# Kernel optimization log

Measured on AMD Instinct MI355X. Metric: run time of the kernel, lower is better.

Reference implementation:

```python
import jax, jax.numpy as jnp
import numpy as np

N = 50000      # nodes
E = 800000     # edges
IN = 128       # in_dim
H = 128        # hidden_dim
OUT = 64       # out_dim
B = 6          # block_num
NEG_SLOPE = 0.01  # nn.LeakyReLU default


def setup_inputs() -> dict:
    key = jax.random.key(0)
    ks = jax.random.split(key, 10)
    s = 0.05
    return {
        "inputs": jax.random.normal(ks[0], (N, IN), jnp.float32),
        "edges": jax.random.randint(ks[1], (2, E), 0, N, jnp.int32),
        "w_in": jax.random.normal(ks[2], (IN, H), jnp.float32) * s,
        "b_in": jnp.zeros((H,), jnp.float32),
        "w1": jax.random.normal(ks[3], (B, H, H), jnp.float32) * s,
        "b1": jnp.zeros((B, H), jnp.float32),
        "w2": jax.random.normal(ks[4], (B, H, H), jnp.float32) * s,
        "b2": jnp.zeros((B, H), jnp.float32),
        "w_out": jax.random.normal(ks[5], (H, OUT), jnp.float32) * s,
        "b_out": jnp.zeros((OUT,), jnp.float32),
    }


def _leaky(x):
    return jnp.where(x >= 0, x, NEG_SLOPE * x)


def _gcn_conv(x, W, b, src, dst, norm):
    # GCNConv: out = D^{-1/2}(A+I)D^{-1/2} (x W) + b, with self-loops folded in.
    xw = x @ W                                   # [N, d_out]
    msg = xw[src] * norm[src, None]              # gather + edge scaling [E, d_out]
    agg = jax.ops.segment_sum(msg, dst, num_segments=N)
    agg = agg * norm[:, None] + xw * (norm * norm)[:, None]  # neighbors + self-loop
    return agg + b


def reference(inputs, edges, w_in, b_in, w1, b1, w2, b2, w_out, b_out):
    src, dst = edges[0], edges[1]
    deg = 1.0 + jax.ops.segment_sum(jnp.ones((E,), inputs.dtype), dst, num_segments=N)
    norm = jax.lax.rsqrt(deg)                    # [N]

    x = _leaky(_gcn_conv(inputs, w_in, b_in, src, dst, norm))
    for i in range(B):  # fixed small layer loop (structurally distinct params)
        h = _leaky(_gcn_conv(x, w1[i], b1[i], src, dst, norm))
        h = _leaky(_gcn_conv(h, w2[i], b2[i], src, dst, norm))
        x = (x + h) * 0.5
    # dropout in eval mode -> identity
    x_out = _gcn_conv(x, w_out, b_out, src, dst, norm)
    return (x_out, x)
```

## Files before the change

### kernel.cpp

```cpp
#include <hip/hip_runtime.h>

#define NNODES 50000
#define NPAD   50048
#define NEDGES 800000
#define HDIM 128
#define OUTDIM 64

#define GEMM_GRID 391
#define GEMM_BLK  512
#define GEMM_TILES (NPAD / 16)

typedef short short8 __attribute__((ext_vector_type(8)));
typedef _Float16 half8 __attribute__((ext_vector_type(8)));
typedef _Float16 half4 __attribute__((ext_vector_type(4)));
typedef float f32x4 __attribute__((ext_vector_type(4)));
typedef float f32x8 __attribute__((ext_vector_type(8)));

__device__ __forceinline__ unsigned short f2bf(float f) {
    unsigned int u = __builtin_bit_cast(unsigned int, f);
    unsigned int r = (u + 0x7FFFu + ((u >> 16) & 1u)) >> 16;
    return (unsigned short)r;
}
__device__ __forceinline__ float bf2f(unsigned short b) {
    unsigned int u = ((unsigned int)b) << 16;
    return __builtin_bit_cast(float, u);
}

__global__ void count_kernel(const int* __restrict__ dst, int* __restrict__ deg,
                             int* __restrict__ epos) {
    int e = blockIdx.x * 256 + threadIdx.x;
    if (e < NEDGES) epos[e] = atomicAdd(&deg[dst[e]], 1);
}

__global__ __launch_bounds__(256) void bsum_kernel(const int* __restrict__ deg,
                                                   int* __restrict__ bsum) {
    __shared__ int red[256];
    int i = blockIdx.x * 256 + threadIdx.x;
    red[threadIdx.x] = (i < NNODES) ? deg[i] : 0;
    __syncthreads();
    for (int off = 128; off; off >>= 1) {
        if (threadIdx.x < off) red[threadIdx.x] += red[threadIdx.x + off];
        __syncthreads();
    }
    if (threadIdx.x == 0) bsum[blockIdx.x] = red[0];
}

__global__ __launch_bounds__(256) void bscan_kernel(const int* __restrict__ bsum,
                                                    int* __restrict__ bofs) {
    __shared__ int s[256];
    int t = threadIdx.x;
    int v = (t < 196) ? bsum[t] : 0;
    s[t] = v;
    __syncthreads();
    for (int off = 1; off < 256; off <<= 1) {
        int u = (t >= off) ? s[t - off] : 0;
        __syncthreads();
        s[t] += u;
        __syncthreads();
    }
    if (t < 196) bofs[t] = s[t] - v;
}

__global__ __launch_bounds__(256) void emit_kernel(
    const int* __restrict__ deg, const int* __restrict__ bofs,
    int* __restrict__ row_ptr, float* __restrict__ norm) {
    __shared__ int s[256];
    int t = threadIdx.x;
    int i = blockIdx.x * 256 + t;
    int v = (i < NNODES) ? deg[i] : 0;
    s[t] = v;
    __syncthreads();
    for (int off = 1; off < 256; off <<= 1) {
        int u = (t >= off) ? s[t - off] : 0;
        __syncthreads();
        s[t] += u;
        __syncthreads();
    }
    int excl = s[t] - v + bofs[blockIdx.x];
    if (i < NNODES) {
        row_ptr[i] = excl;
        norm[i] = rsqrtf(1.0f + (float)v);
    }
    if (i == NNODES - 1) row_ptr[NNODES] = NEDGES;
}

__global__ void fill_kernel(const int* __restrict__ src, const int* __restrict__ dst,
                            const int* __restrict__ epos, const int* __restrict__ row_ptr,
                            int* __restrict__ sorted_src) {
    int e = blockIdx.x * 256 + threadIdx.x;
    if (e < NEDGES) sorted_src[row_ptr[dst[e]] + epos[e]] = src[e];
}

__global__ __launch_bounds__(256) void prep_w_kernel(
    const float* __restrict__ w_in, const float* __restrict__ w1,
    const float* __restrict__ w2, const float* __restrict__ w_out,
    unsigned short* __restrict__ wT, _Float16* __restrict__ w2f) {
    int idx = blockIdx.x * 256 + threadIdx.x;
    if (idx < 16384 + 98304) {
        const float* W;
        unsigned short* o;
        int e;
        if (idx < 16384) {
            W = w_in; o = wT; e = idx;
        } else {
            int j = idx - 16384; int m = j >> 14; e = j & 16383;
            W = w1 + ((size_t)m << 14); o = wT + (size_t)(1 + m) * 32768;
        }
        int k = e >> 7, n = e & 127;
        float v = W[e];
        unsigned short h = f2bf(v);
        o[(size_t)n * 256 + k] = h;
        o[(size_t)n * 256 + 128 + k] = f2bf(v - bf2f(h));
    } else if (idx < 16384 + 196608) {
        int j = idx - 16384 - 98304; int m = j >> 14; int e = j & 16383;
        int k = e >> 7, n = e & 127;
        w2f[(size_t)m * 16384 + n * 128 + k] = (_Float16)w2[((size_t)m << 14) + e];
    } else {
        int e = idx - 212992;
        int k = e >> 6, n = e & 63;
        float v = w_out[e];
        unsigned short h = f2bf(v);
        unsigned short* o = wT + (size_t)7 * 32768;
        o[(size_t)n * 256 + k] = h;
        o[(size_t)n * 256 + 128 + k] = f2bf(v - bf2f(h));
    }
}

__global__ __launch_bounds__(256) void split_x_kernel(
    const float* __restrict__ x, unsigned short* __restrict__ xc) {
    int gid = blockIdx.x * 256 + threadIdx.x;
    int row = gid >> 6;
    int kk = (gid & 63) * 2;
    float2 v = {0.f, 0.f};
    if (row < NNODES) v = *(const float2*)(x + (size_t)row * 128 + kk);
    unsigned short h0 = f2bf(v.x), h1 = f2bf(v.y);
    unsigned short l0 = f2bf(v.x - bf2f(h0)), l1 = f2bf(v.y - bf2f(h1));
    *(unsigned int*)(xc + (size_t)row * 256 + kk) =
        (unsigned int)h0 | ((unsigned int)h1 << 16);
    *(unsigned int*)(xc + (size_t)row * 256 + 128 + kk) =
        (unsigned int)l0 | ((unsigned int)l1 << 16);
}

template <int NCOLS>
__global__ __launch_bounds__(GEMM_BLK) void gemm_bf_kernel(
    const unsigned short* __restrict__ xc, const unsigned short* __restrict__ wT,
    const float* __restrict__ norm, _Float16* __restrict__ y) {
    __shared__ unsigned short Blds[NCOLS * 256];
    const int t = threadIdx.x;
    const int wave = t >> 6, lane = t & 63, quad = lane >> 4, l16 = lane & 15;

    constexpr int NCH = NCOLS * 32;
#pragma unroll
    for (int i = 0; i < NCH / GEMM_BLK; ++i) {
        int C = i * GEMM_BLK + t;
        int n = C >> 5, c = C & 31;
        const unsigned short* gp = wT + ((size_t)n << 8) + ((c ^ (n & 7)) << 3);
        unsigned short* lp = Blds + ((size_t)C << 3);
        __builtin_amdgcn_global_load_lds(
            (const __attribute__((address_space(1))) void*)gp,
            (__attribute__((address_space(3))) void*)lp, 16, 0, 0);
    }
    __syncthreads();

    const int wid = blockIdx.x * (GEMM_BLK / 64) + wave;
    const int sw = l16 & 7;
    const int rb0 = wid * 16;

    short8 a0[8];
    const unsigned short* ap0 = xc + ((size_t)(rb0 + l16) << 8) + quad * 8;
#pragma unroll
    for (int ck = 0; ck < 8; ++ck) a0[ck] = *(const short8*)(ap0 + ck * 32);

    float nm0[4];
#pragma unroll
    for (int r = 0; r < 4; ++r) {
        int r0 = rb0 + quad * 4 + r;
        nm0[r] = norm[r0 < NNODES ? r0 : 0];
    }

#pragma unroll
    for (int nt = 0; nt < NCOLS / 16; ++nt) {
        const unsigned short* bp = Blds + ((size_t)(nt * 16 + l16) << 8);
        short8 bh[4], bl[4];
#pragma unroll
        for (int ck = 0; ck < 4; ++ck) {
            bh[ck] = *(const short8*)(bp + (((ck * 4 + quad) ^ sw) << 3));
            bl[ck] = *(const short8*)(bp + (((16 + ck * 4 + quad) ^ sw) << 3));
        }
        f32x4 ac0 = (f32x4){0.f, 0.f, 0.f, 0.f};
#pragma unroll
        for (int ck = 0; ck < 4; ++ck) {
            ac0 = __builtin_amdgcn_mfma_f32_16x16x32_bf16(a0[ck], bh[ck], ac0, 0, 0, 0);
            ac0 = __builtin_amdgcn_mfma_f32_16x16x32_bf16(a0[ck], bl[ck], ac0, 0, 0, 0);
            ac0 = __builtin_amdgcn_mfma_f32_16x16x32_bf16(a0[4 + ck], bh[ck], ac0, 0, 0, 0);
        }
        int col = nt * 16 + l16;
#pragma unroll
        for (int r = 0; r < 4; ++r) {
            int r0 = rb0 + quad * 4 + r;
            if (r0 < NNODES) y[(size_t)r0 * NCOLS + col] = (_Float16)(ac0[r] * nm0[r]);
        }
    }
}

__global__ __launch_bounds__(GEMM_BLK) void fgg_f16_kernel(
    const _Float16* __restrict__ y, const int* __restrict__ row_ptr,
    const int* __restrict__ sorted_src, const float* __restrict__ norm,
    const float* __restrict__ bias, const _Float16* __restrict__ wf,
    _Float16* __restrict__ yout) {
    __shared__ _Float16 Blds[128 * 128];
    __shared__ _Float16 Alds[8 * 16 * 128];
    const int t = threadIdx.x;
    const int wave = t >> 6, lane = t & 63, quad = lane >> 4, l16 = lane & 15;

#pragma unroll
    for (int i = 0; i < 2048 / GEMM_BLK; ++i) {
        int C = i * GEMM_BLK + t;
        int n = C >> 4, c = C & 15;
        const _Float16* gp = wf + ((size_t)n << 7) + ((c ^ (n & 7)) << 3);
        _Float16* lp = Blds + ((size_t)C << 3);
        __builtin_amdgcn_global_load_lds(
            (const __attribute__((address_space(1))) void*)gp,
            (__attribute__((address_space(3))) void*)lp, 16, 0, 0);
    }

    const int wid = blockIdx.x * (GEMM_BLK / 64) + wave;
    const int rb0 = wid * 16;
    _Float16* Aw = Alds + (size_t)wave * 2048;
    const int g = quad, j = l16;

    for (int tb = 0; tb < 4; ++tb) {
        const int n = rb0 + tb * 4 + g;
        const bool valid = n < NNODES;
        const int beg = valid ? row_ptr[n] : 0;
        const int dg = valid ? (row_ptr[n + 1] - beg) : 0;
        int dmax = dg;
        dmax = max(dmax, __shfl_xor(dmax, 16));
        dmax = max(dmax, __shfl_xor(dmax, 32));

        f32x8 acc = (f32x8){0.f, 0.f, 0.f, 0.f, 0.f, 0.f, 0.f, 0.f};
        for (int i = 0; i < dmax; i += 8) {
            int sarr[8];
#pragma unroll
            for (int u = 0; u < 8; ++u)
                sarr[u] = (i + u < dg) ? sorted_src[beg + i + u] : -1;
            half8 h[8];
#pragma unroll
            for (int u = 0; u < 8; ++u)
                if (sarr[u] >= 0)
                    h[u] = *(const half8*)(y + ((size_t)sarr[u] << 7) + j * 8);
#pragma unroll
            for (int u = 0; u < 8; ++u)
                if (sarr[u] >= 0) acc += __builtin_convertvector(h[u], f32x8);
        }

        half8 o;
        if (valid) {
            const half8 sh = *(const half8*)(y + ((size_t)n << 7) + j * 8);
            const f32x4 b0 = *(const f32x4*)(bias + j * 8);
            const f32x4 b1 = *(const f32x4*)(bias + j * 8 + 4);
            const float bb[8] = {b0[0], b0[1], b0[2], b0[3], b1[0], b1[1], b1[2], b1[3]};
            const float nm = norm[n];
#pragma unroll
            for (int c = 0; c < 8; ++c) {
                float v = (acc[c] + (float)sh[c]) * nm + bb[c];
                v = v >= 0.f ? v : 0.01f * v;
                o[c] = (_Float16)v;
            }
        } else {
#pragma unroll
            for (int c = 0; c < 8; ++c) o[c] = (_Float16)0.f;
        }
        *(half8*)(Aw + (size_t)(tb * 4 + g) * 128 + j * 8) = o;
    }
    __syncthreads();

    const int sw = l16 & 7;
    half8 a0[4];
#pragma unroll
    for (int ck = 0; ck < 4; ++ck)
        a0[ck] = *(const half8*)(Aw + (size_t)l16 * 128 + ck * 32 + quad * 8);

    float nm0[4];
#pragma unroll
    for (int r = 0; r < 4; ++r) {
        int r0 = rb0 + quad * 4 + r;
        nm0[r] = norm[r0 < NNODES ? r0 : 0];
    }

#pragma unroll
    for (int nt = 0; nt < 8; ++nt) {
        const _Float16* bp = Blds + ((size_t)(nt * 16 + l16) << 7);
        half8 b[4];
#pragma unroll
        for (int ck = 0; ck < 4; ++ck)
            b[ck] = *(const half8*)(bp + (((ck * 4 + quad) ^ sw) << 3));
        f32x4 ac0 = (f32x4){0.f, 0.f, 0.f, 0.f};
#pragma unroll
        for (int ck = 0; ck < 4; ++ck)
            ac0 = __builtin_amdgcn_mfma_f32_16x16x32_f16(a0[ck], b[ck], ac0, 0, 0, 0);
        int col = nt * 16 + l16;
#pragma unroll
        for (int r = 0; r < 4; ++r) {
            int r0 = rb0 + quad * 4 + r;
            if (r0 < NNODES) yout[(size_t)r0 * 128 + col] = (_Float16)(ac0[r] * nm0[r]);
        }
    }
}

template <int MODE, bool WOUT, bool OUT16>
__global__ __launch_bounds__(256) void gather_fin128(
    const _Float16* __restrict__ y, const int* __restrict__ row_ptr,
    const int* __restrict__ sorted_src, const float* __restrict__ norm,
    const float* __restrict__ bias, const unsigned short* __restrict__ xcres,
    float* __restrict__ out, unsigned short* __restrict__ xcout,
    _Float16* __restrict__ h16) {
    const int wave = threadIdx.x >> 6;
    const int lane = threadIdx.x & 63;
    const int g = lane >> 4, j = lane & 15;
    const int n = blockIdx.x * 16 + wave * 4 + g;
    const int beg = row_ptr[n];
    const int deg = row_ptr[n + 1] - beg;
    int dmax = deg;
    dmax = max(dmax, __shfl_xor(dmax, 16));
    dmax = max(dmax, __shfl_xor(dmax, 32));

    f32x8 acc = (f32x8){0.f, 0.f, 0.f, 0.f, 0.f, 0.f, 0.f, 0.f};

    for (int i = 0; i < dmax; i += 8) {
        int sarr[8];
#pragma unroll
        for (int u = 0; u < 8; ++u)
            sarr[u] = (i + u < deg) ? sorted_src[beg + i + u] : -1;
        half8 h[8];
#pragma unroll
        for (int u = 0; u < 8; ++u)
            if (sarr[u] >= 0)
                h[u] = *(const half8*)(y + ((size_t)sarr[u] << 7) + j * 8);
#pragma unroll
        for (int u = 0; u < 8; ++u)
            if (sarr[u] >= 0) acc += __builtin_convertvector(h[u], f32x8);
    }

    const half8 sh = *(const half8*)(y + ((size_t)n << 7) + j * 8);
    const f32x4 b0 = *(const f32x4*)(bias + j * 8);
    const f32x4 b1 = *(const f32x4*)(bias + j * 8 + 4);
    const float bb[8] = {b0[0], b0[1], b0[2], b0[3], b1[0], b1[1], b1[2], b1[3]};
    const float nm = norm[n];
    float v[8];
#pragma unroll
    for (int c = 0; c < 8; ++c) {
        float t = (acc[c] + (float)sh[c]) * nm + bb[c];
        v[c] = t >= 0.f ? t : 0.01f * t;
    }
    if (MODE == 1) {
        short8 hw = __builtin_nontemporal_load(
            (const short8*)(xcres + ((size_t)n << 8) + j * 8));
        short8 lw = __builtin_nontemporal_load(
            (const short8*)(xcres + ((size_t)n << 8) + 128 + j * 8));
#pragma unroll
        for (int c = 0; c < 8; ++c) {
            float xr = bf2f((unsigned short)hw[c]) + bf2f((unsigned short)lw[c]);
            v[c] = (xr + v[c]) * 0.5f;
        }
    }
    if (WOUT) {
        f32x4 o0 = (f32x4){v[0], v[1], v[2], v[3]};
        f32x4 o1 = (f32x4){v[4], v[5], v[6], v[7]};
        __builtin_nontemporal_store(o0, (f32x4*)(out + ((size_t)n << 7) + j * 8));
        __builtin_nontemporal_store(o1, (f32x4*)(out + ((size_t)n << 7) + j * 8 + 4));
    }
    if (OUT16) {
        half8 o;
#pragma unroll
        for (int c = 0; c < 8; ++c) o[c] = (_Float16)v[c];
        *(half8*)(h16 + ((size_t)n << 7) + j * 8) = o;
    } else {
        short8 hi, lo;
#pragma unroll
        for (int c = 0; c < 8; ++c) {
            unsigned short hv = f2bf(v[c]);
            hi[c] = (short)hv;
            lo[c] = (short)f2bf(v[c] - bf2f(hv));
        }
        *(short8*)(xcout + ((size_t)n << 8) + j * 8) = hi;
        *(short8*)(xcout + ((size_t)n << 8) + 128 + j * 8) = lo;
    }
}

__global__ __launch_bounds__(256) void gather_fin64(
    const _Float16* __restrict__ y, const int* __restrict__ row_ptr,
    const int* __restrict__ sorted_src, const float* __restrict__ norm,
    const float* __restrict__ bias, float* __restrict__ out) {
    const int wave = threadIdx.x >> 6;
    const int lane = threadIdx.x & 63;
    const int g = lane >> 4, j = lane & 15;
    const int n = blockIdx.x * 16 + wave * 4 + g;
    const int beg = row_ptr[n];
    const int deg = row_ptr[n + 1] - beg;
    int dmax = deg;
    dmax = max(dmax, __shfl_xor(dmax, 16));
    dmax = max(dmax, __shfl_xor(dmax, 32));

    f32x4 acc = (f32x4){0.f, 0.f, 0.f, 0.f};
    for (int i = 0; i < dmax; i += 8) {
        int sarr[8];
#pragma unroll
        for (int u = 0; u < 8; ++u)
            sarr[u] = (i + u < deg) ? sorted_src[beg + i + u] : -1;
        half4 h[8];
#pragma unroll
        for (int u = 0; u < 8; ++u)
            if (sarr[u] >= 0)
                h[u] = *(const half4*)(y + ((size_t)sarr[u] << 6) + j * 4);
#pragma unroll
        for (int u = 0; u < 8; ++u)
            if (sarr[u] >= 0) acc += __builtin_convertvector(h[u], f32x4);
    }

    const half4 sh = *(const half4*)(y + ((size_t)n << 6) + j * 4);
    const f32x4 b = *(const f32x4*)(bias + j * 4);
    const float nm = norm[n];
    f32x4 o;
    o[0] = (acc[0] + (float)sh[0]) * nm + b[0];
    o[1] = (acc[1] + (float)sh[1]) * nm + b[1];
    o[2] = (acc[2] + (float)sh[2]) * nm + b[2];
    o[3] = (acc[3] + (float)sh[3]) * nm + b[3];
    __builtin_nontemporal_store(o, (f32x4*)(out + ((size_t)n << 6) + j * 4));
}

extern "C" void kernel_launch(void* const* d_in, const int* in_sizes, int n_in,
                              void* d_out, int out_size, void* d_ws, size_t ws_size,
                              hipStream_t stream) {
    const float* inputs = (const float*)d_in[0];
    const int* edges = (const int*)d_in[1];
    const int* src = edges;
    const int* dst = edges + NEDGES;
    const float* w_in  = (const float*)d_in[2];
    const float* b_in  = (const float*)d_in[3];
    const float* w1    = (const float*)d_in[4];
    const float* b1    = (const float*)d_in[5];
    const float* w2    = (const float*)d_in[6];
    const float* b2    = (const float*)d_in[7];
    const float* w_out = (const float*)d_in[8];
    const float* b_out = (const float*)d_in[9];

    float* out  = (float*)d_out;
    float* xout = out;
    float* x    = out + (size_t)NNODES * OUTDIM;

    char* p = (char*)d_ws;
    auto alloc = [&](size_t bytes) {
        char* r = p;
        p += (bytes + 63) & ~(size_t)63;
        return r;
    };
    int* deg        = (int*)alloc(NNODES * 4);
    int* epos       = (int*)alloc(NEDGES * 4);
    int* row_ptr    = (int*)alloc((NNODES + 1) * 4);
    int* bsum       = (int*)alloc(256 * 4);
    int* bofs       = (int*)alloc(256 * 4);
    int* sorted_src = (int*)alloc(NEDGES * 4);
    float* normb    = (float*)alloc(NNODES * 4);
    unsigned short* wT = (unsigned short*)alloc((size_t)245760 * 2);
    _Float16* w2f   = (_Float16*)alloc((size_t)6 * 16384 * 2);
    unsigned short* xc_x = (unsigned short*)alloc((size_t)NPAD * 256 * 2);
    unsigned short* xc_in = (unsigned short*)alloc((size_t)NPAD * 256 * 2);
    _Float16* y2    = (_Float16*)alloc((size_t)NPAD * 128 * 2);
    _Float16* y     = (_Float16*)alloc((size_t)NNODES * HDIM * 2);

    hipMemsetAsync(deg, 0, NNODES * sizeof(int), stream);
    count_kernel<<<(NEDGES + 255) / 256, 256, 0, stream>>>(dst, deg, epos);
    bsum_kernel<<<196, 256, 0, stream>>>(deg, bsum);
    bscan_kernel<<<1, 256, 0, stream>>>(bsum, bofs);
    emit_kernel<<<196, 256, 0, stream>>>(deg, bofs, row_ptr, normb);
    fill_kernel<<<(NEDGES + 255) / 256, 256, 0, stream>>>(src, dst, epos, row_ptr, sorted_src);
    prep_w_kernel<<<864, 256, 0, stream>>>(w_in, w1, w2, w_out, wT, w2f);

    split_x_kernel<<<(NPAD * 64) / 256, 256, 0, stream>>>(inputs, xc_in);
    gemm_bf_kernel<128><<<GEMM_GRID, GEMM_BLK, 0, stream>>>(xc_in, wT, normb, y);
    gather_fin128<0, false, false><<<NNODES / 16, 256, 0, stream>>>(
        y, row_ptr, sorted_src, normb, b_in, nullptr, nullptr, xc_x, nullptr);

    for (int i = 0; i < 6; ++i) {
        gemm_bf_kernel<128><<<GEMM_GRID, GEMM_BLK, 0, stream>>>(
            xc_x, wT + (size_t)(1 + i) * 32768, normb, y);
        fgg_f16_kernel<<<GEMM_GRID, GEMM_BLK, 0, stream>>>(
            y, row_ptr, sorted_src, normb, b1 + i * HDIM,
            w2f + (size_t)i * 16384, y2);
        if (i < 5)
            gather_fin128<1, false, false><<<NNODES / 16, 256, 0, stream>>>(
                y2, row_ptr, sorted_src, normb, b2 + i * HDIM, xc_x, nullptr, xc_x, nullptr);
        else
            gather_fin128<1, true, false><<<NNODES / 16, 256, 0, stream>>>(
                y2, row_ptr, sorted_src, normb, b2 + i * HDIM, xc_x, x, xc_x, nullptr);
    }

    gemm_bf_kernel<64><<<GEMM_GRID, GEMM_BLK, 0, stream>>>(
        xc_x, wT + (size_t)7 * 32768, normb, y);
    gather_fin64<<<NNODES / 16, 256, 0, stream>>>(
        y, row_ptr, sorted_src, normb, b_out, xout);
}
```

Measured before the change: 742.6 us.

## Fuse residual gather/finalize with next layer's split-bf16 GEMM

Adds an fgb_kernel that performs the neighbor gather, bias, LeakyReLU and residual averaging for a 16-row tile, writes the split bf16 hi/lo residual, then immediately runs the next layer's bf16 MFMA GEMM on the tile held in LDS. This removes the separate gemm_bf_kernel launches and the global round trip of reading xc_x back for each subsequent GEMM, including the final output projection. It also moves the __syncthreads in fgg_f16 to right after the weight LDS load. In exchange each block needs more LDS (a 128x256 weight tile plus an A tile) and more registers, which may reduce occupancy for the gather phase.

```diff
diff --git a/kernel.cpp b/kernel.cpp
--- a/kernel.cpp
+++ b/kernel.cpp
@@ -8,7 +8,6 @@
 
 #define GEMM_GRID 391
 #define GEMM_BLK  512
-#define GEMM_TILES (NPAD / 16)
 
 typedef short short8 __attribute__((ext_vector_type(8)));
 typedef _Float16 half8 __attribute__((ext_vector_type(8)));
@@ -203,6 +202,145 @@
     }
 }
 
+template <int MODE, int NCOLS, bool WOUT, bool WRXC>
+__global__ __launch_bounds__(GEMM_BLK) void fgb_kernel(
+    const _Float16* __restrict__ y, const int* __restrict__ row_ptr,
+    const int* __restrict__ sorted_src, const float* __restrict__ norm,
+    const float* __restrict__ bias, const unsigned short* __restrict__ xcres,
+    const unsigned short* __restrict__ wTb, unsigned short* __restrict__ xcout,
+    float* __restrict__ xfull, _Float16* __restrict__ yout) {
+    __shared__ unsigned short Blds[NCOLS * 256];
+    __shared__ unsigned short Alds[8 * 16 * 256];
+    const int t = threadIdx.x;
+    const int wave = t >> 6, lane = t & 63, quad = lane >> 4, l16 = lane & 15;
+
+    constexpr int NCH = NCOLS * 32;
+#pragma unroll
+    for (int i = 0; i < NCH / GEMM_BLK; ++i) {
+        int C = i * GEMM_BLK + t;
+        int n = C >> 5, c = C & 31;
+        const unsigned short* gp = wTb + ((size_t)n << 8) + ((c ^ (n & 7)) << 3);
+        unsigned short* lp = Blds + ((size_t)C << 3);
+        __builtin_amdgcn_global_load_lds(
+            (const __attribute__((address_space(1))) void*)gp,
+            (__attribute__((address_space(3))) void*)lp, 16, 0, 0);
+    }
+    __syncthreads();
+
+    const int wid = blockIdx.x * (GEMM_BLK / 64) + wave;
+    const int rb0 = wid * 16;
+    unsigned short* Aw = Alds + (size_t)wave * 4096;
+    const int g = quad, j = l16;
+
+    for (int tb = 0; tb < 4; ++tb) {
+        const int n = rb0 + tb * 4 + g;
+        const bool valid = n < NNODES;
+        const int beg = valid ? row_ptr[n] : 0;
+        const int dg = valid ? (row_ptr[n + 1] - beg) : 0;
+        int dmax = dg;
+        dmax = max(dmax, __shfl_xor(dmax, 16));
+        dmax = max(dmax, __shfl_xor(dmax, 32));
+
+        f32x8 acc = (f32x8){0.f, 0.f, 0.f, 0.f, 0.f, 0.f, 0.f, 0.f};
+        for (int i = 0; i < dmax; i += 8) {
+            int sarr[8];
+#pragma unroll
+            for (int u = 0; u < 8; ++u)
+                sarr[u] = (i + u < dg) ? sorted_src[beg + i + u] : -1;
+            half8 h[8];
+#pragma unroll
+            for (int u = 0; u < 8; ++u)
+                if (sarr[u] >= 0)
+                    h[u] = *(const half8*)(y + ((size_t)sarr[u] << 7) + j * 8);
+#pragma unroll
+            for (int u = 0; u < 8; ++u)
+                if (sarr[u] >= 0) acc += __builtin_convertvector(h[u], f32x8);
+        }
+
+        short8 hi = (short8){0, 0, 0, 0, 0, 0, 0, 0};
+        short8 lo = hi;
+        if (valid) {
+            const half8 sh = *(const half8*)(y + ((size_t)n << 7) + j * 8);
+            const f32x4 b0 = *(const f32x4*)(bias + j * 8);
+            const f32x4 b1 = *(const f32x4*)(bias + j * 8 + 4);
+            const float bb[8] = {b0[0], b0[1], b0[2], b0[3], b1[0], b1[1], b1[2], b1[3]};
+            const float nm = norm[n];
+            float v[8];
+#pragma unroll
+            for (int c = 0; c < 8; ++c) {
+                float tv = (acc[c] + (float)sh[c]) * nm + bb[c];
+                v[c] = tv >= 0.f ? tv : 0.01f * tv;
+            }
+            if (MODE == 1) {
+                short8 hw = __builtin_nontemporal_load(
+                    (const short8*)(xcres + ((size_t)n << 8) + j * 8));
+                short8 lw = __builtin_nontemporal_load(
+                    (const short8*)(xcres + ((size_t)n << 8) + 128 + j * 8));
+#pragma unroll
+                for (int c = 0; c < 8; ++c) {
+                    float xr = bf2f((unsigned short)hw[c]) + bf2f((unsigned short)lw[c]);
+                    v[c] = (xr + v[c]) * 0.5f;
+                }
+            }
+            if (WOUT) {
+                f32x4 o0 = (f32x4){v[0], v[1], v[2], v[3]};
+                f32x4 o1 = (f32x4){v[4], v[5], v[6], v[7]};
+                __builtin_nontemporal_store(o0, (f32x4*)(xfull + ((size_t)n << 7) + j * 8));
+                __builtin_nontemporal_store(o1, (f32x4*)(xfull + ((size_t)n << 7) + j * 8 + 4));
+            }
+#pragma unroll
+            for (int c = 0; c < 8; ++c) {
+                unsigned short hv = f2bf(v[c]);
+                hi[c] = (short)hv;
+                lo[c] = (short)f2bf(v[c] - bf2f(hv));
+            }
+            if (WRXC) {
+                *(short8*)(xcout + ((size_t)n << 8) + j * 8) = hi;
+                *(short8*)(xcout + ((size_t)n << 8) + 128 + j * 8) = lo;
+            }
+        }
+        *(short8*)(Aw + (size_t)(tb * 4 + g) * 256 + j * 8) = hi;
+        *(short8*)(Aw + (size_t)(tb * 4 + g) * 256 + 128 + j * 8) = lo;
+    }
+
+    const int sw = l16 & 7;
+    short8 a0[8];
+#pragma unroll
+    for (int ck = 0; ck < 8; ++ck)
+        a0[ck] = *(const short8*)(Aw + (size_t)l16 * 256 + quad * 8 + ck * 32);
+
+    float nm0[4];
+#pragma unroll
+    for (int r = 0; r < 4; ++r) {
+        int r0 = rb0 + quad * 4 + r;
+        nm0[r] = norm[r0 < NNODES ? r0 : 0];
+    }
+
+#pragma unroll
+    for (int nt = 0; nt < NCOLS / 16; ++nt) {
+        const unsigned short* bp = Blds + ((size_t)(nt * 16 + l16) << 8);
+        short8 bh[4], bl[4];
+#pragma unroll
+        for (int ck = 0; ck < 4; ++ck) {
+            bh[ck] = *(const short8*)(bp + (((ck * 4 + quad) ^ sw) << 3));
+            bl[ck] = *(const short8*)(bp + (((16 + ck * 4 + quad) ^ sw) << 3));
+        }
+        f32x4 ac0 = (f32x4){0.f, 0.f, 0.f, 0.f};
+#pragma unroll
+        for (int ck = 0; ck < 4; ++ck) {
+            ac0 = __builtin_amdgcn_mfma_f32_16x16x32_bf16(a0[ck], bh[ck], ac0, 0, 0, 0);
+            ac0 = __builtin_amdgcn_mfma_f32_16x16x32_bf16(a0[ck], bl[ck], ac0, 0, 0, 0);
+            ac0 = __builtin_amdgcn_mfma_f32_16x16x32_bf16(a0[4 + ck], bh[ck], ac0, 0, 0, 0);
+        }
+        int col = nt * 16 + l16;
+#pragma unroll
+        for (int r = 0; r < 4; ++r) {
+            int r0 = rb0 + quad * 4 + r;
+            if (r0 < NNODES) yout[(size_t)r0 * NCOLS + col] = (_Float16)(ac0[r] * nm0[r]);
+        }
+    }
+}
+
 __global__ __launch_bounds__(GEMM_BLK) void fgg_f16_kernel(
     const _Float16* __restrict__ y, const int* __restrict__ row_ptr,
     const int* __restrict__ sorted_src, const float* __restrict__ norm,
@@ -223,6 +361,7 @@
             (const __attribute__((address_space(1))) void*)gp,
             (__attribute__((address_space(3))) void*)lp, 16, 0, 0);
     }
+    __syncthreads();
 
     const int wid = blockIdx.x * (GEMM_BLK / 64) + wave;
     const int rb0 = wid * 16;
@@ -273,7 +412,6 @@
         }
         *(half8*)(Aw + (size_t)(tb * 4 + g) * 128 + j * 8) = o;
     }
-    __syncthreads();
 
     const int sw = l16 & 7;
     half8 a0[4];
@@ -305,86 +443,6 @@
             int r0 = rb0 + quad * 4 + r;
             if (r0 < NNODES) yout[(size_t)r0 * 128 + col] = (_Float16)(ac0[r] * nm0[r]);
         }
-    }
-}
-
-template <int MODE, bool WOUT, bool OUT16>
-__global__ __launch_bounds__(256) void gather_fin128(
-    const _Float16* __restrict__ y, const int* __restrict__ row_ptr,
-    const int* __restrict__ sorted_src, const float* __restrict__ norm,
-    const float* __restrict__ bias, const unsigned short* __restrict__ xcres,
-    float* __restrict__ out, unsigned short* __restrict__ xcout,
-    _Float16* __restrict__ h16) {
-    const int wave = threadIdx.x >> 6;
-    const int lane = threadIdx.x & 63;
-    const int g = lane >> 4, j = lane & 15;
-    const int n = blockIdx.x * 16 + wave * 4 + g;
-    const int beg = row_ptr[n];
-    const int deg = row_ptr[n + 1] - beg;
-    int dmax = deg;
-    dmax = max(dmax, __shfl_xor(dmax, 16));
-    dmax = max(dmax, __shfl_xor(dmax, 32));
-
-    f32x8 acc = (f32x8){0.f, 0.f, 0.f, 0.f, 0.f, 0.f, 0.f, 0.f};
-
-    for (int i = 0; i < dmax; i += 8) {
-        int sarr[8];
-#pragma unroll
-        for (int u = 0; u < 8; ++u)
-            sarr[u] = (i + u < deg) ? sorted_src[beg + i + u] : -1;
-        half8 h[8];
-#pragma unroll
-        for (int u = 0; u < 8; ++u)
-            if (sarr[u] >= 0)
-                h[u] = *(const half8*)(y + ((size_t)sarr[u] << 7) + j * 8);
-#pragma unroll
-        for (int u = 0; u < 8; ++u)
-            if (sarr[u] >= 0) acc += __builtin_convertvector(h[u], f32x8);
-    }
-
-    const half8 sh = *(const half8*)(y + ((size_t)n << 7) + j * 8);
-    const f32x4 b0 = *(const f32x4*)(bias + j * 8);
-    const f32x4 b1 = *(const f32x4*)(bias + j * 8 + 4);
-    const float bb[8] = {b0[0], b0[1], b0[2], b0[3], b1[0], b1[1], b1[2], b1[3]};
-    const float nm = norm[n];
-    float v[8];
-#pragma unroll
-    for (int c = 0; c < 8; ++c) {
-        float t = (acc[c] + (float)sh[c]) * nm + bb[c];
-        v[c] = t >= 0.f ? t : 0.01f * t;
-    }
-    if (MODE == 1) {
-        short8 hw = __builtin_nontemporal_load(
-            (const short8*)(xcres + ((size_t)n << 8) + j * 8));
-        short8 lw = __builtin_nontemporal_load(
-            (const short8*)(xcres + ((size_t)n << 8) + 128 + j * 8));
-#pragma unroll
-        for (int c = 0; c < 8; ++c) {
-            float xr = bf2f((unsigned short)hw[c]) + bf2f((unsigned short)lw[c]);
-            v[c] = (xr + v[c]) * 0.5f;
-        }
-    }
-    if (WOUT) {
-        f32x4 o0 = (f32x4){v[0], v[1], v[2], v[3]};
-        f32x4 o1 = (f32x4){v[4], v[5], v[6], v[7]};
-        __builtin_nontemporal_store(o0, (f32x4*)(out + ((size_t)n << 7) + j * 8));
-        __builtin_nontemporal_store(o1, (f32x4*)(out + ((size_t)n << 7) + j * 8 + 4));
-    }
-    if (OUT16) {
-        half8 o;
-#pragma unroll
-        for (int c = 0; c < 8; ++c) o[c] = (_Float16)v[c];
-        *(half8*)(h16 + ((size_t)n << 7) + j * 8) = o;
-    } else {
-        short8 hi, lo;
-#pragma unroll
-        for (int c = 0; c < 8; ++c) {
-            unsigned short hv = f2bf(v[c]);
-            hi[c] = (short)hv;
-            lo[c] = (short)f2bf(v[c] - bf2f(hv));
-        }
-        *(short8*)(xcout + ((size_t)n << 8) + j * 8) = hi;
-        *(short8*)(xcout + ((size_t)n << 8) + 128 + j * 8) = lo;
     }
 }
 
@@ -466,8 +524,8 @@
     _Float16* w2f   = (_Float16*)alloc((size_t)6 * 16384 * 2);
     unsigned short* xc_x = (unsigned short*)alloc((size_t)NPAD * 256 * 2);
     unsigned short* xc_in = (unsigned short*)alloc((size_t)NPAD * 256 * 2);
-    _Float16* y2    = (_Float16*)alloc((size_t)NPAD * 128 * 2);
-    _Float16* y     = (_Float16*)alloc((size_t)NNODES * HDIM * 2);
+    _Float16* Ya    = (_Float16*)alloc((size_t)NPAD * 128 * 2);
+    _Float16* Yb    = (_Float16*)alloc((size_t)NPAD * 128 * 2);
 
     hipMemsetAsync(deg, 0, NNODES * sizeof(int), stream);
     count_kernel<<<(NEDGES + 255) / 256, 256, 0, stream>>>(dst, deg, epos);
@@ -478,26 +536,25 @@
     prep_w_kernel<<<864, 256, 0, stream>>>(w_in, w1, w2, w_out, wT, w2f);
 
     split_x_kernel<<<(NPAD * 64) / 256, 256, 0, stream>>>(inputs, xc_in);
-    gemm_bf_kernel<128><<<GEMM_GRID, GEMM_BLK, 0, stream>>>(xc_in, wT, normb, y);
-    gather_fin128<0, false, false><<<NNODES / 16, 256, 0, stream>>>(
-        y, row_ptr, sorted_src, normb, b_in, nullptr, nullptr, xc_x, nullptr);
+    gemm_bf_kernel<128><<<GEMM_GRID, GEMM_BLK, 0, stream>>>(xc_in, wT, normb, Ya);
+    fgb_kernel<0, 128, false, true><<<GEMM_GRID, GEMM_BLK, 0, stream>>>(
+        Ya, row_ptr, sorted_src, normb, b_in, nullptr,
+        wT + (size_t)1 * 32768, xc_x, nullptr, Yb);
 
     for (int i = 0; i < 6; ++i) {
-        gemm_bf_kernel<128><<<GEMM_GRID, GEMM_BLK, 0, stream>>>(
-            xc_x, wT + (size_t)(1 + i) * 32768, normb, y);
         fgg_f16_kernel<<<GEMM_GRID, GEMM_BLK, 0, stream>>>(
-            y, row_ptr, sorted_src, normb, b1 + i * HDIM,
-            w2f + (size_t)i * 16384, y2);
+            Yb, row_ptr, sorted_src, normb, b1 + i * HDIM,
+            w2f + (size_t)i * 16384, Ya);
         if (i < 5)
-            gather_fin128<1, false, false><<<NNODES / 16, 256, 0, stream>>>(
-                y2, row_ptr, sorted_src, normb, b2 + i * HDIM, xc_x, nullptr, xc_x, nullptr);
+            fgb_kernel<1, 128, false, true><<<GEMM_GRID, GEMM_BLK, 0, stream>>>(
+                Ya, row_ptr, sorted_src, normb, b2 + i * HDIM, xc_x,
+                wT + (size_t)(2 + i) * 32768, xc_x, nullptr, Yb);
         else
-            gather_fin128<1, true, false><<<NNODES / 16, 256, 0, stream>>>(
-                y2, row_ptr, sorted_src, normb, b2 + i * HDIM, xc_x, x, xc_x, nullptr);
-    }
-
-    gemm_bf_kernel<64><<<GEMM_GRID, GEMM_BLK, 0, stream>>>(
-        xc_x, wT + (size_t)7 * 32768, normb, y);
+            fgb_kernel<1, 64, true, false><<<GEMM_GRID, GEMM_BLK, 0, stream>>>(
+                Ya, row_ptr, sorted_src, normb, b2 + i * HDIM, xc_x,
+                wT + (size_t)7 * 32768, nullptr, x, Yb);
+    }
+
     gather_fin64<<<NNODES / 16, 256, 0, stream>>>(
-        y, row_ptr, sorted_src, normb, b_out, xout);
-}
+        Yb, row_ptr, sorted_src, normb, b_out, xout);
+}
```

New measurement: 841.0 us. 1.13x slower.

## Sort nodes by degree within 16-node groups to balance wave gather loops

Applied to the files above, without the earlier changes.

Adds a kernel that, inside each 16-node group, orders nodes by descending in-degree and writes a permutation. The gather and fused gather-GEMM kernels process nodes through this permutation, so the four nodes sharing a wave have similar degrees and the loop bound set by the largest degree wastes fewer iterations. In exchange, output row writes are scattered within each group and every kernel does one extra indirection load. The LDS barrier in the fused kernel also moves to right after the async weight load, while the previous barrier before the per-wave A-tile read is dropped.

```diff
diff --git a/kernel.cpp b/kernel.cpp
--- a/kernel.cpp
+++ b/kernel.cpp
@@ -8,7 +8,6 @@
 
 #define GEMM_GRID 391
 #define GEMM_BLK  512
-#define GEMM_TILES (NPAD / 16)
 
 typedef short short8 __attribute__((ext_vector_type(8)));
 typedef _Float16 half8 __attribute__((ext_vector_type(8)));
@@ -89,6 +88,27 @@
                             int* __restrict__ sorted_src) {
     int e = blockIdx.x * 256 + threadIdx.x;
     if (e < NEDGES) sorted_src[row_ptr[dst[e]] + epos[e]] = src[e];
+}
+
+__global__ __launch_bounds__(256) void dsort16_kernel(
+    const int* __restrict__ deg, int* __restrict__ perm) {
+    __shared__ int dl[256];
+    int t = threadIdx.x;
+    int i = blockIdx.x * 256 + t;
+    int d = (i < NNODES) ? deg[i] : -1;
+    dl[t] = d;
+    __syncthreads();
+    if (i < NPAD) {
+        int wbase = t & ~15;
+        int s = t & 15;
+        int rank = 0;
+#pragma unroll
+        for (int k = 0; k < 16; ++k) {
+            int dk = dl[wbase + k];
+            rank += (dk > d) || (dk == d && k < s);
+        }
+        perm[blockIdx.x * 256 + wbase + rank] = i;
+    }
 }
 
 __global__ __launch_bounds__(256) void prep_w_kernel(
@@ -207,7 +227,7 @@
     const _Float16* __restrict__ y, const int* __restrict__ row_ptr,
     const int* __restrict__ sorted_src, const float* __restrict__ norm,
     const float* __restrict__ bias, const _Float16* __restrict__ wf,
-    _Float16* __restrict__ yout) {
+    _Float16* __restrict__ yout, const int* __restrict__ perm) {
     __shared__ _Float16 Blds[128 * 128];
     __shared__ _Float16 Alds[8 * 16 * 128];
     const int t = threadIdx.x;
@@ -223,6 +243,7 @@
             (const __attribute__((address_space(1))) void*)gp,
             (__attribute__((address_space(3))) void*)lp, 16, 0, 0);
     }
+    __syncthreads();
 
     const int wid = blockIdx.x * (GEMM_BLK / 64) + wave;
     const int rb0 = wid * 16;
@@ -230,7 +251,7 @@
     const int g = quad, j = l16;
 
     for (int tb = 0; tb < 4; ++tb) {
-        const int n = rb0 + tb * 4 + g;
+        const int n = perm[rb0 + tb * 4 + g];
         const bool valid = n < NNODES;
         const int beg = valid ? row_ptr[n] : 0;
         const int dg = valid ? (row_ptr[n + 1] - beg) : 0;
@@ -273,7 +294,6 @@
         }
         *(half8*)(Aw + (size_t)(tb * 4 + g) * 128 + j * 8) = o;
     }
-    __syncthreads();
 
     const int sw = l16 & 7;
     half8 a0[4];
@@ -281,11 +301,13 @@
     for (int ck = 0; ck < 4; ++ck)
         a0[ck] = *(const half8*)(Aw + (size_t)l16 * 128 + ck * 32 + quad * 8);
 
+    int pr[4];
     float nm0[4];
 #pragma unroll
     for (int r = 0; r < 4; ++r) {
-        int r0 = rb0 + quad * 4 + r;
-        nm0[r] = norm[r0 < NNODES ? r0 : 0];
+        int p = perm[rb0 + quad * 4 + r];
+        pr[r] = p;
+        nm0[r] = norm[p < NNODES ? p : 0];
     }
 
 #pragma unroll
@@ -302,8 +324,8 @@
         int col = nt * 16 + l16;
 #pragma unroll
         for (int r = 0; r < 4; ++r) {
-            int r0 = rb0 + quad * 4 + r;
-            if (r0 < NNODES) yout[(size_t)r0 * 128 + col] = (_Float16)(ac0[r] * nm0[r]);
+            if (pr[r] < NNODES)
+                yout[(size_t)pr[r] * 128 + col] = (_Float16)(ac0[r] * nm0[r]);
         }
     }
 }
@@ -314,11 +336,11 @@
     const int* __restrict__ sorted_src, const float* __restrict__ norm,
     const float* __restrict__ bias, const unsigned short* __restrict__ xcres,
     float* __restrict__ out, unsigned short* __restrict__ xcout,
-    _Float16* __restrict__ h16) {
+    _Float16* __restrict__ h16, const int* __restrict__ perm) {
     const int wave = threadIdx.x >> 6;
     const int lane = threadIdx.x & 63;
     const int g = lane >> 4, j = lane & 15;
-    const int n = blockIdx.x * 16 + wave * 4 + g;
+    const int n = perm[blockIdx.x * 16 + wave * 4 + g];
     const int beg = row_ptr[n];
     const int deg = row_ptr[n + 1] - beg;
     int dmax = deg;
@@ -391,11 +413,12 @@
 __global__ __launch_bounds__(256) void gather_fin64(
     const _Float16* __restrict__ y, const int* __restrict__ row_ptr,
     const int* __restrict__ sorted_src, const float* __restrict__ norm,
-    const float* __restrict__ bias, float* __restrict__ out) {
+    const float* __restrict__ bias, float* __restrict__ out,
+    const int* __restrict__ perm) {
     const int wave = threadIdx.x >> 6;
     const int lane = threadIdx.x & 63;
     const int g = lane >> 4, j = lane & 15;
-    const int n = blockIdx.x * 16 + wave * 4 + g;
+    const int n = perm[blockIdx.x * 16 + wave * 4 + g];
     const int beg = row_ptr[n];
     const int deg = row_ptr[n + 1] - beg;
     int dmax = deg;
@@ -462,6 +485,7 @@
     int* bofs       = (int*)alloc(256 * 4);
     int* sorted_src = (int*)alloc(NEDGES * 4);
     float* normb    = (float*)alloc(NNODES * 4);
+    int* perm       = (int*)alloc(NPAD * 4);
     unsigned short* wT = (unsigned short*)alloc((size_t)245760 * 2);
     _Float16* w2f   = (_Float16*)alloc((size_t)6 * 16384 * 2);
     unsigned short* xc_x = (unsigned short*)alloc((size_t)NPAD * 256 * 2);
@@ -471,6 +495,7 @@
 
     hipMemsetAsync(deg, 0, NNODES * sizeof(int), stream);
     count_kernel<<<(NEDGES + 255) / 256, 256, 0, stream>>>(dst, deg, epos);
+    dsort16_kernel<<<196, 256, 0, stream>>>(deg, perm);
     bsum_kernel<<<196, 256, 0, stream>>>(deg, bsum);
     bscan_kernel<<<1, 256, 0, stream>>>(bsum, bofs);
     emit_kernel<<<196, 256, 0, stream>>>(deg, bofs, row_ptr, normb);
@@ -480,24 +505,24 @@
     split_x_kernel<<<(NPAD * 64) / 256, 256, 0, stream>>>(inputs, xc_in);
     gemm_bf_kernel<128><<<GEMM_GRID, GEMM_BLK, 0, stream>>>(xc_in, wT, normb, y);
     gather_fin128<0, false, false><<<NNODES / 16, 256, 0, stream>>>(
-        y, row_ptr, sorted_src, normb, b_in, nullptr, nullptr, xc_x, nullptr);
+        y, row_ptr, sorted_src, normb, b_in, nullptr, nullptr, xc_x, nullptr, perm);
 
     for (int i = 0; i < 6; ++i) {
         gemm_bf_kernel<128><<<GEMM_GRID, GEMM_BLK, 0, stream>>>(
             xc_x, wT + (size_t)(1 + i) * 32768, normb, y);
         fgg_f16_kernel<<<GEMM_GRID, GEMM_BLK, 0, stream>>>(
             y, row_ptr, sorted_src, normb, b1 + i * HDIM,
-            w2f + (size_t)i * 16384, y2);
+            w2f + (size_t)i * 16384, y2, perm);
         if (i < 5)
             gather_fin128<1, false, false><<<NNODES / 16, 256, 0, stream>>>(
-                y2, row_ptr, sorted_src, normb, b2 + i * HDIM, xc_x, nullptr, xc_x, nullptr);
+                y2, row_ptr, sorted_src, normb, b2 + i * HDIM, xc_x, nullptr, xc_x, nullptr, perm);
         else
             gather_fin128<1, true, false><<<NNODES / 16, 256, 0, stream>>>(
-                y2, row_ptr, sorted_src, normb, b2 + i * HDIM, xc_x, x, xc_x, nullptr);
+                y2, row_ptr, sorted_src, normb, b2 + i * HDIM, xc_x, x, xc_x, nullptr, perm);
     }
 
     gemm_bf_kernel<64><<<GEMM_GRID, GEMM_BLK, 0, stream>>>(
         xc_x, wT + (size_t)7 * 32768, normb, y);
     gather_fin64<<<NNODES / 16, 256, 0, stream>>>(
-        y, row_ptr, sorted_src, normb, b_out, xout);
-}
+        y, row_ptr, sorted_src, normb, b_out, xout, perm);
+}
```

New measurement: 746.1 us. About the same (+0.5%).
